# Optimization experiments

Measured on AMD Instinct MI355X. Metric: run time of the kernel, lower is better.

Reference implementation:

```python
import jax, jax.numpy as jnp
import numpy as np
from jax import lax

ALPHA = 4.0  # spikingjelly default Sigmoid surrogate alpha
EPS = 1e-5

@jax.custom_vjp
def spike_fn(u):
    return (u >= 0.0).astype(u.dtype)

def _spike_fwd(u):
    return spike_fn(u), u

def _spike_bwd(u, g):
    sg = jax.nn.sigmoid(ALPHA * u)
    return (g * ALPHA * sg * (1.0 - sg),)

spike_fn.defvjp(_spike_fwd, _spike_bwd)

def if_node(x):
    """Multi-step IF neuron (v_threshold=1, hard reset to 0) over leading T dim."""
    def step(v, xt):
        v = v + xt
        s = spike_fn(v - 1.0)
        v = v * (1.0 - s)
        return v, s
    _, spikes = lax.scan(step, jnp.zeros_like(x[0]), x)
    return spikes

def layer_norm(x, g, b):
    m = jnp.mean(x, axis=-1, keepdims=True)
    var = jnp.mean((x - m) ** 2, axis=-1, keepdims=True)
    return (x - m) * lax.rsqrt(var + EPS) * g + b

def setup_inputs() -> dict:
    key = jax.random.key(0)
    T, B, S, D = 4, 8, 1024, 768
    ks = jax.random.split(key, 5)
    scale = 1.0 / np.sqrt(D)
    inp = {
        "x": jax.random.normal(ks[0], (T, B, S, D), jnp.float32),
        "wq": jax.random.normal(ks[1], (D, D), jnp.float32) * scale,
        "wk": jax.random.normal(ks[2], (D, D), jnp.float32) * scale,
        "wv": jax.random.normal(ks[3], (D, D), jnp.float32) * scale,
        "wo": jax.random.normal(ks[4], (D, D), jnp.float32) * scale,
        "gq": jnp.ones((D,), jnp.float32), "bq": jnp.zeros((D,), jnp.float32),
        "gk": jnp.ones((D,), jnp.float32), "bk": jnp.zeros((D,), jnp.float32),
        "gv": jnp.ones((D,), jnp.float32), "bv": jnp.zeros((D,), jnp.float32),
        "go": jnp.ones((D,), jnp.float32), "bo": jnp.zeros((D,), jnp.float32),
    }
    return inp

def reference(x, wq, wk, wv, wo, gq, bq, gk, bk, gv, bv, go, bo):
    T, B, S, D = x.shape
    H, HD = 12, 64
    tmp = if_node(x)                                   # [T,B,S,D] spikes
    Q = if_node(layer_norm(tmp @ wq, gq, bq))
    K = if_node(layer_norm(tmp @ wk, gk, bk))
    V = if_node(layer_norm(tmp @ wv, gv, bv))
    # [T,B,S,H,HD] -> [T,B,H,S,HD]
    Q = Q.reshape(T, B, S, H, HD).transpose(0, 1, 3, 2, 4)
    K = K.reshape(T, B, S, H, HD).transpose(0, 1, 3, 2, 4)
    V = V.reshape(T, B, S, H, HD).transpose(0, 1, 3, 2, 4)
    QK = jnp.sum(Q * K, axis=-2, keepdims=True)        # [T,B,H,1,HD]
    QK = if_node(QK)                                   # talking_heads IF spikes
    QKV = V * QK                                       # broadcast over S
    QKV = QKV.transpose(0, 1, 3, 2, 4).reshape(T, B, S, D)
    return layer_norm(QKV @ wo, go, bo)
```

## Files before the change

### kernel.cpp

```cpp
#include <hip/hip_runtime.h>
#include <hip/hip_bf16.h>

#define T_ 4
#define B_ 8
#define S_ 1024
#define D_ 768
#define BS_ (B_*S_)
#define M_ (T_*B_*S_)
#define BSD_ (B_*S_*D_)
#define LN_EPS 1e-5f
#define TAU 4e-5f
#define TAU2 2e-6f
#define ECAP (1 << 20)

typedef unsigned short u16;
typedef unsigned char u8;
typedef unsigned int u32;
typedef unsigned long long u64;
typedef __bf16 bf16x8 __attribute__((ext_vector_type(8)));
typedef float f32x4 __attribute__((ext_vector_type(4)));

__global__ __launch_bounds__(768)
void k_if_mask(const float* __restrict__ x, u64* __restrict__ Am2) {
    int bs = blockIdx.x;
    int d = threadIdx.x;
    int wv = d >> 6, lane = d & 63;
    float v = 0.f;
    for (int t = 0; t < T_; ++t) {
        v += x[(size_t)t * BSD_ + (size_t)bs * D_ + d];
        bool s = (v >= 1.0f);
        u64 m = __ballot(s);
        if (lane == 0) Am2[((size_t)t * BS_ + bs) * 12 + wv] = m;
        if (s) v = 0.f;
    }
}

__global__ void k_wconv(const float* __restrict__ wq, const float* __restrict__ wk,
                        const float* __restrict__ wv, const float* __restrict__ wo,
                        u16* __restrict__ Whi, u16* __restrict__ Wlo, u16* __restrict__ Wo) {
    int idx = blockIdx.x * 256 + threadIdx.x;
    int mat = idx / (D_ * D_);
    int r = idx % (D_ * D_);
    int n = r / D_;
    int k = r % D_;
    const float* src = (mat == 0) ? wq : (mat == 1) ? wk : (mat == 2) ? wv : wo;
    float w = src[k * D_ + n];
    __bf16 hi = (__bf16)w;
    u16 uhi = __builtin_bit_cast(u16, hi);
    if (mat == 3) { Wo[r] = uhi; return; }
    float lo = w - (float)hi;
    u16 ulo = __builtin_bit_cast(u16, (__bf16)lo);
    Whi[(size_t)mat * D_ * D_ + r] = uhi;
    Wlo[(size_t)mat * D_ * D_ + r] = ulo;
}

__device__ __forceinline__ void gload16(const void* g, void* l) {
    __builtin_amdgcn_global_load_lds(
        (const __attribute__((address_space(1))) unsigned int*)g,
        (__attribute__((address_space(3))) unsigned int*)l, 16, 0, 0);
}

template<int NMATS, int KSTEP>
__global__ __launch_bounds__(256)
void k_gemm(const u64* __restrict__ Amask_g,
            const u16* __restrict__ Bh0, const u16* __restrict__ Bl0, float* __restrict__ C0,
            const u16* __restrict__ Bh1, const u16* __restrict__ Bl1, float* __restrict__ C1,
            const u16* __restrict__ Bh2, const u16* __restrict__ Bl2, float* __restrict__ C2,
            int ntn, int N) {
    constexpr int CH = KSTEP / 8;
    constexpr int CMASK = CH - 1;
    constexpr int NSUB = KSTEP / 32;
    constexpr int NW64 = KSTEP / 64;
    constexpr int NLOAD = KSTEP / 16;
    __shared__ __align__(16) u16 Bh[128 * KSTEP];
    __shared__ __align__(16) u16 Bl[NMATS == 2 ? 128 * KSTEP : 8];
    __shared__ __align__(16) u64 Amsk[128 * 13];
    __shared__ __align__(16) u32 LUT[256 * 4];
    int my = blockIdx.y;
    const u16* Bhi = (my == 0) ? Bh0 : (my == 1) ? Bh1 : Bh2;
    const u16* Blo = (my == 0) ? Bl0 : (my == 1) ? Bl1 : Bl2;
    float* C = (my == 0) ? C0 : (my == 1) ? C1 : C2;
    int bid = blockIdx.x;
    bid = (bid & 7) * (gridDim.x >> 3) + (bid >> 3);
    int bn = bid % ntn, bm = bid / ntn;
    int tid = threadIdx.x;
    int l = tid & 63, w = tid >> 6;
    int wr = w >> 1, wc = w & 1;
    int lan16 = l & 15, kh = l >> 4;

    {
        int e = tid;
        LUT[e * 4 + 0] = (((e >> 0) & 1) ? 0x3F80u : 0u) | (((e >> 1) & 1) ? 0x3F800000u : 0u);
        LUT[e * 4 + 1] = (((e >> 2) & 1) ? 0x3F80u : 0u) | (((e >> 3) & 1) ? 0x3F800000u : 0u);
        LUT[e * 4 + 2] = (((e >> 4) & 1) ? 0x3F80u : 0u) | (((e >> 5) & 1) ? 0x3F800000u : 0u);
        LUT[e * 4 + 3] = (((e >> 6) & 1) ? 0x3F80u : 0u) | (((e >> 7) & 1) ? 0x3F800000u : 0u);
    }
    #pragma unroll
    for (int j = 0; j < 6; ++j) {
        int idx = tid + j * 256;
        int r = idx / 12, kw = idx % 12;
        Amsk[r * 13 + kw] = Amask_g[(size_t)(bm * 128 + r) * 12 + kw];
    }

    f32x4 acc[4][4];
    #pragma unroll
    for (int m = 0; m < 4; ++m)
        #pragma unroll
        for (int n = 0; n < 4; ++n)
            #pragma unroll
            for (int r = 0; r < 4; ++r) acc[m][n][r] = 0.f;

    int srow[NLOAD], scol[NLOAD];
    #pragma unroll
    for (int j = 0; j < NLOAD; ++j) {
        int li = j * 256 + tid;
        srow[j] = li / CH;
        scol[j] = ((li & CMASK) ^ ((li / CH) & CMASK)) * 8;
    }
    int wbase = (tid >> 6) << 10;

    int arow[4], boff[4][NSUB];
    #pragma unroll
    for (int m = 0; m < 4; ++m) arow[m] = (wr * 64 + m * 16 + lan16) * 13;
    #pragma unroll
    for (int n = 0; n < 4; ++n)
        #pragma unroll
        for (int s = 0; s < NSUB; ++s) {
            int Rb = wc * 64 + n * 16 + lan16;
            boff[n][s] = Rb * (KSTEP * 2) + (((s * 4 + kh) ^ (Rb & CMASK)) << 4);
        }
    const char* LUTb = (const char*)LUT;

    for (int step = 0; step < 768 / KSTEP; ++step) {
        int kk = step * KSTEP;
        #pragma unroll
        for (int j = 0; j < NLOAD; ++j) {
            gload16(Bhi + (size_t)(bn * 128 + srow[j]) * 768 + kk + scol[j],
                    (char*)Bh + j * 4096 + wbase);
            if (NMATS == 2)
                gload16(Blo + (size_t)(bn * 128 + srow[j]) * 768 + kk + scol[j],
                        (char*)Bl + j * 4096 + wbase);
        }
        __syncthreads();
        u64 mA[4][NW64];
        #pragma unroll
        for (int m = 0; m < 4; ++m)
            #pragma unroll
            for (int ww = 0; ww < NW64; ++ww)
                mA[m][ww] = Amsk[arow[m] + step * NW64 + ww];
        #pragma unroll
        for (int s = 0; s < NSUB; ++s) {
            bf16x8 af[4], bh[4], bl[4];
            #pragma unroll
            for (int m = 0; m < 4; ++m) {
                int bitpos = s * 32;
                u64 mw = mA[m][bitpos >> 6];
                u32 byt = (u32)(mw >> ((bitpos & 63) + kh * 8)) & 0xFFu;
                af[m] = *(const bf16x8*)(LUTb + byt * 16);
            }
            #pragma unroll
            for (int n = 0; n < 4; ++n) {
                bh[n] = *(const bf16x8*)((const char*)Bh + boff[n][s]);
                if (NMATS == 2) bl[n] = *(const bf16x8*)((const char*)Bl + boff[n][s]);
            }
            #pragma unroll
            for (int m = 0; m < 4; ++m)
                #pragma unroll
                for (int n = 0; n < 4; ++n) {
                    acc[m][n] = __builtin_amdgcn_mfma_f32_16x16x32_bf16(af[m], bh[n], acc[m][n], 0, 0, 0);
                    if (NMATS == 2)
                        acc[m][n] = __builtin_amdgcn_mfma_f32_16x16x32_bf16(af[m], bl[n], acc[m][n], 0, 0, 0);
                }
        }
        __syncthreads();
    }
    #pragma unroll
    for (int m = 0; m < 4; ++m)
        #pragma unroll
        for (int n = 0; n < 4; ++n)
            #pragma unroll
            for (int r = 0; r < 4; ++r) {
                int crow = bm * 128 + wr * 64 + m * 16 + kh * 4 + r;
                int ccol = bn * 128 + wc * 64 + n * 16 + lan16;
                C[(size_t)crow * N + ccol] = acc[m][n][r];
            }
}

__global__ __launch_bounds__(256)
void k_lnif(const float* __restrict__ Y0, const float* __restrict__ Y1,
            const float* __restrict__ Y2,
            const float* __restrict__ gq, const float* __restrict__ bq,
            const float* __restrict__ gk, const float* __restrict__ bk,
            const float* __restrict__ gv, const float* __restrict__ bv,
            u8* __restrict__ Qs, u8* __restrict__ Ks, u8* __restrict__ Vs,
            float2* __restrict__ MI, u32* __restrict__ elist, int* __restrict__ ecnt,
            int mat0) {
    #pragma clang fp contract(off)
    int mat = mat0 + blockIdx.y;
    const float* Y = (mat == 0) ? Y0 : (mat == 1) ? Y1 : Y2;
    const float* g = (mat == 0) ? gq : (mat == 1) ? gk : gv;
    const float* bt = (mat == 0) ? bq : (mat == 1) ? bk : bv;
    u8* Sp = (mat == 0) ? Qs : (mat == 1) ? Ks : Vs;
    int row = blockIdx.x * 4 + (threadIdx.x >> 6);
    int lane = threadIdx.x & 63;
    float v[12];
    bool fl[12];
    #pragma unroll
    for (int i = 0; i < 12; ++i) { v[i] = 0.f; fl[i] = false; }
    float gv_[12], bv_[12];
    #pragma unroll
    for (int i = 0; i < 12; ++i) { gv_[i] = g[lane + 64*i]; bv_[i] = bt[lane + 64*i]; }
    for (int t = 0; t < T_; ++t) {
        size_t base = ((size_t)t * BS_ + row) * D_;
        float xv[12];
        double s = 0.0;
        #pragma unroll
        for (int i = 0; i < 12; ++i) { xv[i] = Y[base + lane + 64*i]; s += (double)xv[i]; }
        #pragma unroll
        for (int o = 1; o < 64; o <<= 1) s += __shfl_xor(s, o, 64);
        s = __shfl(s, 0, 64);
        float m = (float)(s / 768.0);
        float d[12];
        double q = 0.0;
        #pragma unroll
        for (int i = 0; i < 12; ++i) { d[i] = xv[i] - m; float sq = d[i]*d[i]; q += (double)sq; }
        #pragma unroll
        for (int o = 1; o < 64; o <<= 1) q += __shfl_xor(q, o, 64);
        q = __shfl(q, 0, 64);
        float var = (float)(q / 768.0);
        float inv = 1.0f / __fsqrt_rn(var + LN_EPS);
        if (lane == 0) MI[((size_t)mat * 4 + t) * BS_ + row] = make_float2(m, inv);
        #pragma unroll
        for (int i = 0; i < 12; ++i) {
            float yn = ((d[i] * inv) * gv_[i]) + bv_[i];
            v[i] += yn;
            fl[i] = fl[i] || (fabsf(v[i] - 1.0f) < TAU);
            bool sp = (v[i] >= 1.0f);
            Sp[base + lane + 64*i] = sp ? (u8)1 : (u8)0;
            if (sp) v[i] = 0.f;
        }
    }
    #pragma unroll
    for (int i = 0; i < 12; ++i) {
        if (fl[i]) {
            int slot = atomicAdd(ecnt, 1);
            if (slot < ECAP)
                elist[slot] = ((u32)mat << 23) | ((u32)row << 10) | (u32)(lane + 64*i);
        }
    }
}

__global__ __launch_bounds__(256)
void k_repair2(const u64* __restrict__ Am2,
               const float* __restrict__ wq, const float* __restrict__ wk,
               const float* __restrict__ wv, const float2* __restrict__ MI,
               const float* __restrict__ gq, const float* __restrict__ bq,
               const float* __restrict__ gk, const float* __restrict__ bk,
               const float* __restrict__ gv, const float* __restrict__ bv,
               u8* __restrict__ Qs, u8* __restrict__ Ks, u8* __restrict__ Vs,
               const u32* __restrict__ elist, const int* __restrict__ ecnt,
               int* __restrict__ rowlist2, int* __restrict__ cnt2) {
    #pragma clang fp contract(off)
    int nf = *ecnt;
    if (nf > ECAP) nf = ECAP;
    int t = threadIdx.x & 3;
    int gid = (blockIdx.x * 256 + threadIdx.x) >> 2;
    int ngroups = (gridDim.x * 256) >> 2;
    int lane = threadIdx.x & 63;
    int gbase = lane & ~3;
    for (int e = gid; e < nf; e += ngroups) {
        u32 p = elist[e];
        int mat = p >> 23;
        int row = (p >> 10) & 0x1FFF;
        int col = p & 0x3FF;
        const float* W = (mat == 0) ? wq : (mat == 1) ? wk : wv;
        const float* g = (mat == 0) ? gq : (mat == 1) ? gk : gv;
        const float* bb = (mat == 0) ? bq : (mat == 1) ? bk : bv;
        u8* Sp = (mat == 0) ? Qs : (mat == 1) ? Ks : Vs;
        float y = 0.f;
        for (int kw = 0; kw < 12; ++kw) {
            u64 m = Am2[((size_t)t * BS_ + row) * 12 + kw];
            const float* wp = W + (size_t)(kw * 64) * D_ + col;
            #pragma unroll 16
            for (int kb = 0; kb < 64; ++kb) {
                float w = wp[(size_t)kb * D_];
                y += ((m >> kb) & 1ull) ? w : 0.0f;
            }
        }
        float y0 = __shfl(y, gbase + 0, 64);
        float y1 = __shfl(y, gbase + 1, 64);
        float y2 = __shfl(y, gbase + 2, 64);
        float y3 = __shfl(y, gbase + 3, 64);
        float yt[4] = {y0, y1, y2, y3};
        float gc = g[col], bc = bb[col];
        float v = 0.f;
        bool efl = false;
        #pragma unroll
        for (int tt = 0; tt < 4; ++tt) {
            float2 mi = MI[((size_t)mat * 4 + tt) * BS_ + row];
            float yn = (((yt[tt] - mi.x) * mi.y) * gc) + bc;
            v += yn;
            efl = efl || (fabsf(v - 1.0f) < TAU2);
            bool sp = (v >= 1.0f);
            if (tt == t)
                Sp[((size_t)tt * BS_ + row) * D_ + col] = sp ? (u8)1 : (u8)0;
            if (sp) v = 0.f;
        }
        if (efl && t == 0) {
            int slot = atomicAdd(cnt2 + mat, 1);
            rowlist2[mat * BS_ + slot] = row;
        }
    }
}

__global__ __launch_bounds__(768)
void k_repairT(const u64* __restrict__ Am2,
               const float* __restrict__ wq, const float* __restrict__ wk,
               const float* __restrict__ wv,
               const float* __restrict__ gq, const float* __restrict__ bq,
               const float* __restrict__ gk, const float* __restrict__ bk,
               const float* __restrict__ gv, const float* __restrict__ bv,
               u8* __restrict__ Qs, u8* __restrict__ Ks, u8* __restrict__ Vs,
               const int* __restrict__ rowlist, const int* __restrict__ cnt) {
    #pragma clang fp contract(off)
    int mat = blockIdx.y;
    int nf = cnt[mat];
    const float* W = (mat == 0) ? wq : (mat == 1) ? wk : wv;
    const float* g = (mat == 0) ? gq : (mat == 1) ? gk : gv;
    const float* bb = (mat == 0) ? bq : (mat == 1) ? bk : bv;
    u8* Sp = (mat == 0) ? Qs : (mat == 1) ? Ks : Vs;
    const float4* Wv4 = (const float4*)W;

    __shared__ u64 mks[4][12];
    __shared__ int pops[4][12];
    __shared__ int cnt4[4];
    __shared__ u16 idxs[4][768];
    __shared__ float4 ys[4][192];
    __shared__ float2 mi_sh[4];
    __shared__ double redd[12];

    int tid = threadIdx.x;
    int t = tid / 192;
    int tg = tid % 192;

    for (int e = blockIdx.x; e < nf; e += gridDim.x) {
        int row = rowlist[mat * BS_ + e];

        if (tid < 48) {
            int tt = tid / 12, kw = tid % 12;
            u64 m = Am2[((size_t)tt * BS_ + row) * 12 + kw];
            mks[tt][kw] = m;
            pops[tt][kw] = __popcll(m);
        }
        __syncthreads();
        if (tid < 48) {
            int tt = tid / 12, kw = tid % 12;
            int off = 0;
            for (int j = 0; j < kw; ++j) off += pops[tt][j];
            u64 m = mks[tt][kw];
            int kb0 = kw * 64;
            while (m) {
                int kb = __builtin_ctzll(m);
                m &= m - 1;
                idxs[tt][off++] = (u16)(kb0 + kb);
            }
            if (kw == 11) cnt4[tt] = off;
        }
        __syncthreads();

        int cn = cnt4[t];
        float y0 = 0.f, y1 = 0.f, y2 = 0.f, y3 = 0.f;
        const u16* il = idxs[t];
        #pragma unroll 8
        for (int i = 0; i < cn; ++i) {
            float4 w = Wv4[(size_t)il[i] * 192 + tg];
            y0 += w.x; y1 += w.y; y2 += w.z; y3 += w.w;
        }

        int lane = tid & 63;
        int wv_t = tg >> 6;
        double s = (double)y0 + (double)y1 + (double)y2 + (double)y3;
        #pragma unroll
        for (int o = 1; o < 64; o <<= 1) s += __shfl_xor(s, o, 64);
        if (lane == 0) redd[t * 3 + wv_t] = s;
        __syncthreads();
        double stot = redd[t * 3] + redd[t * 3 + 1] + redd[t * 3 + 2];
        float mean = (float)(stot / 768.0);
        float d0 = y0 - mean, d1 = y1 - mean, d2 = y2 - mean, d3 = y3 - mean;
        double q = (double)(d0*d0) + (double)(d1*d1) + (double)(d2*d2) + (double)(d3*d3);
        #pragma unroll
        for (int o = 1; o < 64; o <<= 1) q += __shfl_xor(q, o, 64);
        __syncthreads();
        if (lane == 0) redd[t * 3 + wv_t] = q;
        __syncthreads();
        double qtot = redd[t * 3] + redd[t * 3 + 1] + redd[t * 3 + 2];
        float var = (float)(qtot / 768.0);
        float inv = 1.0f / __fsqrt_rn(var + LN_EPS);

        ys[t][tg] = make_float4(y0, y1, y2, y3);
        if (tg == 0) mi_sh[t] = make_float2(mean, inv);
        __syncthreads();

        if (tid < 192) {
            float4 gd = ((const float4*)g)[tg];
            float4 bd = ((const float4*)bb)[tg];
            float4 yt[4];
            float2 mi[4];
            #pragma unroll
            for (int tt = 0; tt < 4; ++tt) { yt[tt] = ys[tt][tg]; mi[tt] = mi_sh[tt]; }
            uchar4 o4[4];
            #pragma unroll
            for (int j = 0; j < 4; ++j) {
                float gj = (j == 0) ? gd.x : (j == 1) ? gd.y : (j == 2) ? gd.z : gd.w;
                float bj = (j == 0) ? bd.x : (j == 1) ? bd.y : (j == 2) ? bd.z : bd.w;
                float v = 0.f;
                #pragma unroll
                for (int tt = 0; tt < 4; ++tt) {
                    float yj = (j == 0) ? yt[tt].x : (j == 1) ? yt[tt].y : (j == 2) ? yt[tt].z : yt[tt].w;
                    float d = yj - mi[tt].x;
                    float yn = ((d * mi[tt].y) * gj) + bj;
                    v += yn;
                    bool sp = (v >= 1.0f);
                    u8 sb = sp ? (u8)1 : (u8)0;
                    if (j == 0) o4[tt].x = sb;
                    if (j == 1) o4[tt].y = sb;
                    if (j == 2) o4[tt].z = sb;
                    if (j == 3) o4[tt].w = sb;
                    if (sp) v = 0.f;
                }
            }
            #pragma unroll
            for (int tt = 0; tt < 4; ++tt)
                *(uchar4*)(Sp + ((size_t)tt * BS_ + row) * D_ + tg * 4) = o4[tt];
        }
        __syncthreads();
    }
}

__global__ void k_qkred(const u8* __restrict__ Q, const u8* __restrict__ K,
                        float* __restrict__ QK) {
    int bid = blockIdx.x;
    int sg = bid & 31, tb = bid >> 5;
    int tid = threadIdx.x;
    int c4 = tid * 4;
    size_t base = (size_t)tb * S_ * D_ + (size_t)sg * 32 * D_;
    int acc[4] = {0, 0, 0, 0};
    for (int s = 0; s < 32; ++s) {
        uchar4 q = *(const uchar4*)(Q + base + (size_t)s * D_ + c4);
        uchar4 k = *(const uchar4*)(K + base + (size_t)s * D_ + c4);
        acc[0] += q.x & k.x; acc[1] += q.y & k.y; acc[2] += q.z & k.z; acc[3] += q.w & k.w;
    }
    float* dst = QK + (size_t)tb * D_ + c4;
    #pragma unroll
    for (int j = 0; j < 4; ++j) atomicAdd(dst + j, (float)acc[j]);
}

__global__ __launch_bounds__(768)
void k_qkvm(const u8* __restrict__ Vs, const float* __restrict__ QK,
            u64* __restrict__ Am3) {
    int row = blockIdx.x;
    int d = threadIdx.x;
    int wv = d >> 6, lane = d & 63;
    int t = row >> 13;
    int b = (row & (BS_ - 1)) >> 10;
    float v = 0.f;
    u8 sp_t = 0;
    #pragma unroll
    for (int tt = 0; tt < T_; ++tt) {
        v += QK[tt * (B_ * D_) + b * D_ + d];
        bool s = (v >= 1.0f);
        if (tt == t) sp_t = s ? 1 : 0;
        if (s) v = 0.f;
    }
    u8 vv = Vs[(size_t)row * D_ + d] & sp_t;
    u64 m = __ballot(vv != 0);
    if (lane == 0) Am3[(size_t)row * 12 + wv] = m;
}

__device__ __forceinline__ float block_sum(float v, float* red) {
    #pragma unroll
    for (int o = 32; o > 0; o >>= 1) v += __shfl_down(v, o, 64);
    int lane = threadIdx.x & 63, w = threadIdx.x >> 6;
    __syncthreads();
    if (lane == 0) red[w] = v;
    __syncthreads();
    return (red[0] + red[1]) + (red[2] + red[3]);
}

__global__ __launch_bounds__(256)
void k_lnfinal(const float* __restrict__ Y, const float* __restrict__ g,
               const float* __restrict__ bt, float* __restrict__ out) {
    #pragma clang fp contract(off)
    __shared__ float red[4];
    size_t row = (size_t)blockIdx.x * D_;
    int tid = threadIdx.x;
    float y[3];
    float s = 0.f;
    #pragma unroll
    for (int j = 0; j < 3; ++j) { y[j] = Y[row + tid + j * 256]; s += y[j]; }
    float mean = block_sum(s, red) / 768.0f;
    float q = 0.f;
    #pragma unroll
    for (int j = 0; j < 3; ++j) { float d = y[j] - mean; q += d * d; }
    float var = block_sum(q, red) / 768.0f;
    float inv = 1.0f / __fsqrt_rn(var + LN_EPS);
    #pragma unroll
    for (int j = 0; j < 3; ++j) {
        int c = tid + j * 256;
        out[row + c] = (y[j] - mean) * inv * g[c] + bt[c];
    }
}

extern "C" void kernel_launch(void* const* d_in, const int* in_sizes, int n_in,
                              void* d_out, int out_size, void* d_ws, size_t ws_size,
                              hipStream_t stream) {
    const float* x  = (const float*)d_in[0];
    const float* wq = (const float*)d_in[1];
    const float* wk = (const float*)d_in[2];
    const float* wv = (const float*)d_in[3];
    const float* wo = (const float*)d_in[4];
    const float* gq = (const float*)d_in[5];
    const float* bq = (const float*)d_in[6];
    const float* gk = (const float*)d_in[7];
    const float* bk = (const float*)d_in[8];
    const float* gv = (const float*)d_in[9];
    const float* bv = (const float*)d_in[10];
    const float* go = (const float*)d_in[11];
    const float* bo = (const float*)d_in[12];
    float* out = (float*)d_out;

    char* ws = (char*)d_ws;
    size_t off = 0;
    auto alloc = [&](size_t bytes) -> void* {
        void* p = ws + off;
        off += (bytes + 255) & ~(size_t)255;
        return p;
    };
    u64* Am2   = (u64*)alloc((size_t)M_ * 12 * 8);
    u64* Am3   = (u64*)alloc((size_t)M_ * 12 * 8);
    float* Y0  = (float*)alloc((size_t)M_ * D_ * 4);
    u8* Qs     = (u8*)alloc((size_t)M_ * D_);
    u8* Ks     = (u8*)alloc((size_t)M_ * D_);
    u8* Vs     = (u8*)alloc((size_t)M_ * D_);
    u16* Whi   = (u16*)alloc((size_t)3 * D_ * D_ * 2);
    u16* Wlo   = (u16*)alloc((size_t)3 * D_ * D_ * 2);
    u16* Wo    = (u16*)alloc((size_t)D_ * D_ * 2);
    float* QK  = (float*)alloc((size_t)T_ * B_ * D_ * 4);
    float2* MI = (float2*)alloc((size_t)3 * 4 * BS_ * 8);
    u32* elist = (u32*)alloc((size_t)ECAP * 4);
    int* rowlist2 = (int*)alloc((size_t)3 * BS_ * 4);
    int* cnt   = (int*)alloc(256);
    float* Y1  = (float*)alloc((size_t)M_ * D_ * 4);
    float* Y2  = (float*)alloc((size_t)M_ * D_ * 4);
    bool fused = (off <= ws_size);
    if (!fused) { Y1 = Y0; Y2 = Y0; }
    int* cnt2 = cnt;
    int* ecnt = cnt + 3;

    hipMemsetAsync(QK, 0, (size_t)T_ * B_ * D_ * 4, stream);
    hipMemsetAsync(cnt, 0, 256, stream);

    k_if_mask<<<BS_, 768, 0, stream>>>(x, Am2);
    k_wconv<<<(4 * D_ * D_) / 256, 256, 0, stream>>>(wq, wk, wv, wo, Whi, Wlo, Wo);
    const int ntn = D_ / 128;
    const int gemm_grid = (M_ / 128) * ntn;
    const u16* WhiQ = Whi + 0 * D_ * D_; const u16* WloQ = Wlo + 0 * D_ * D_;
    const u16* WhiK = Whi + 1 * D_ * D_; const u16* WloK = Wlo + 1 * D_ * D_;
    const u16* WhiV = Whi + 2 * D_ * D_; const u16* WloV = Wlo + 2 * D_ * D_;
    if (fused) {
        k_gemm<2, 64><<<dim3(gemm_grid, 3), 256, 0, stream>>>(Am2,
            WhiQ, WloQ, Y0, WhiK, WloK, Y1, WhiV, WloV, Y2, ntn, D_);
        k_lnif<<<dim3(BS_ / 4, 3), 256, 0, stream>>>(Y0, Y1, Y2,
            gq, bq, gk, bk, gv, bv, Qs, Ks, Vs, MI, elist, ecnt, 0);
    } else {
        k_gemm<2, 64><<<dim3(gemm_grid, 1), 256, 0, stream>>>(Am2,
            WhiQ, WloQ, Y0, WhiQ, WloQ, Y0, WhiQ, WloQ, Y0, ntn, D_);
        k_lnif<<<dim3(BS_ / 4, 1), 256, 0, stream>>>(Y0, Y0, Y0,
            gq, bq, gk, bk, gv, bv, Qs, Ks, Vs, MI, elist, ecnt, 0);
        k_gemm<2, 64><<<dim3(gemm_grid, 1), 256, 0, stream>>>(Am2,
            WhiK, WloK, Y0, WhiK, WloK, Y0, WhiK, WloK, Y0, ntn, D_);
        k_lnif<<<dim3(BS_ / 4, 1), 256, 0, stream>>>(Y0, Y0, Y0,
            gq, bq, gk, bk, gv, bv, Qs, Ks, Vs, MI, elist, ecnt, 1);
        k_gemm<2, 64><<<dim3(gemm_grid, 1), 256, 0, stream>>>(Am2,
            WhiV, WloV, Y0, WhiV, WloV, Y0, WhiV, WloV, Y0, ntn, D_);
        k_lnif<<<dim3(BS_ / 4, 1), 256, 0, stream>>>(Y0, Y0, Y0,
            gq, bq, gk, bk, gv, bv, Qs, Ks, Vs, MI, elist, ecnt, 2);
    }
    k_repair2<<<512, 256, 0, stream>>>(Am2, wq, wk, wv, MI, gq, bq, gk, bk, gv, bv,
                                       Qs, Ks, Vs, elist, ecnt, rowlist2, cnt2);
    k_repairT<<<dim3(256, 3), 768, 0, stream>>>(Am2, wq, wk, wv, gq, bq, gk, bk, gv, bv,
                                                Qs, Ks, Vs, rowlist2, cnt2);
    k_qkred<<<T_ * B_ * 32, 192, 0, stream>>>(Qs, Ks, QK);
    k_qkvm<<<M_, 768, 0, stream>>>(Vs, QK, Am3);
    k_gemm<1, 128><<<dim3(gemm_grid, 1), 256, 0, stream>>>(Am3,
        Wo, Wo, Y0, Wo, Wo, Y0, Wo, Wo, Y0, ntn, D_);
    k_lnfinal<<<M_, 256, 0, stream>>>(Y0, go, bo, out);
}
```

Before: 584.5 us.

## Fuse QKV spike GEMM with layernorm and IF neuron in one kernel

Replaces the separate QKV GEMM plus layernorm/IF kernels with one kernel. Each block computes 64 rows (16 tokens × 4 timesteps, enabled by reordering the spike mask layout to token-major) across the full 768 columns. Row statistics and IF spiking are done in registers, so the three fp32 intermediate Y tensors are never written to or read back from global memory. The cost is a large LDS tile (96 KB for B), 512-thread blocks with heavy accumulator register use, and hi/lo weight passes run sequentially, which may lower occupancy.

```diff
diff --git a/kernel.cpp b/kernel.cpp
--- a/kernel.cpp
+++ b/kernel.cpp
@@ -30,7 +30,7 @@
         v += x[(size_t)t * BSD_ + (size_t)bs * D_ + d];
         bool s = (v >= 1.0f);
         u64 m = __ballot(s);
-        if (lane == 0) Am2[((size_t)t * BS_ + bs) * 12 + wv] = m;
+        if (lane == 0) Am2[((size_t)bs * 4 + t) * 12 + wv] = m;
         if (s) v = 0.f;
     }
 }
@@ -60,26 +60,216 @@
         (__attribute__((address_space(3))) unsigned int*)l, 16, 0, 0);
 }
 
-template<int NMATS, int KSTEP>
+__global__ __launch_bounds__(512)
+void k_gemmln(const u64* __restrict__ Am2,
+              const u16* __restrict__ Whi_all, const u16* __restrict__ Wlo_all,
+              const float* __restrict__ gq, const float* __restrict__ bq,
+              const float* __restrict__ gk, const float* __restrict__ bk,
+              const float* __restrict__ gv, const float* __restrict__ bv,
+              u8* __restrict__ Qs, u8* __restrict__ Ks, u8* __restrict__ Vs,
+              float2* __restrict__ MI, u32* __restrict__ elist, int* __restrict__ ecnt) {
+    #pragma clang fp contract(off)
+    __shared__ __align__(16) u16 Bt[768 * 64];
+    __shared__ __align__(16) u64 Amsk[64 * 13];
+    __shared__ __align__(16) u32 LUT[256 * 4];
+    __shared__ double red[64][4];
+    int mat = blockIdx.y;
+    const u16* Bhi = Whi_all + (size_t)mat * D_ * D_;
+    const u16* Blo = Wlo_all + (size_t)mat * D_ * D_;
+    const float* g = (mat == 0) ? gq : (mat == 1) ? gk : gv;
+    const float* bt = (mat == 0) ? bq : (mat == 1) ? bk : bv;
+    u8* Sp = (mat == 0) ? Qs : (mat == 1) ? Ks : Vs;
+
+    int bid = blockIdx.x;
+    bid = (bid & 7) * (gridDim.x >> 3) + (bid >> 3);
+    int bm = bid;
+    int tid = threadIdx.x;
+    int wid = tid >> 6, l = tid & 63;
+    int rh = wid >> 2, cq = wid & 3;
+    int lan16 = l & 15, kh = l >> 4;
+
+    if (tid < 256) {
+        int e = tid;
+        LUT[e * 4 + 0] = (((e >> 0) & 1) ? 0x3F80u : 0u) | (((e >> 1) & 1) ? 0x3F800000u : 0u);
+        LUT[e * 4 + 1] = (((e >> 2) & 1) ? 0x3F80u : 0u) | (((e >> 3) & 1) ? 0x3F800000u : 0u);
+        LUT[e * 4 + 2] = (((e >> 4) & 1) ? 0x3F80u : 0u) | (((e >> 5) & 1) ? 0x3F800000u : 0u);
+        LUT[e * 4 + 3] = (((e >> 6) & 1) ? 0x3F80u : 0u) | (((e >> 7) & 1) ? 0x3F800000u : 0u);
+    }
+    {
+        int idx = tid;
+        if (idx < 768) {
+            int r = idx / 12, kw = idx % 12;
+            Amsk[r * 13 + kw] = Am2[(size_t)(bm * 64 + r) * 12 + kw];
+        }
+        idx = tid + 512;
+        if (idx < 768) {
+            int r = idx / 12, kw = idx % 12;
+            Amsk[r * 13 + kw] = Am2[(size_t)(bm * 64 + r) * 12 + kw];
+        }
+    }
+
+    f32x4 acc[2][12];
+    #pragma unroll
+    for (int fm = 0; fm < 2; ++fm)
+        #pragma unroll
+        for (int fn = 0; fn < 12; ++fn)
+            #pragma unroll
+            for (int r = 0; r < 4; ++r) acc[fm][fn][r] = 0.f;
+
+    int srow[12], scol[12];
+    #pragma unroll
+    for (int j = 0; j < 12; ++j) {
+        int li = j * 512 + tid;
+        srow[j] = li >> 3;
+        scol[j] = ((li & 7) ^ ((li >> 3) & 7)) * 8;
+    }
+    int wbase = wid << 10;
+
+    int arow[2], boff[12][2];
+    #pragma unroll
+    for (int fm = 0; fm < 2; ++fm) arow[fm] = (rh * 32 + fm * 16 + lan16) * 13;
+    #pragma unroll
+    for (int fn = 0; fn < 12; ++fn)
+        #pragma unroll
+        for (int ss = 0; ss < 2; ++ss) {
+            int n = cq * 192 + fn * 16 + lan16;
+            boff[fn][ss] = n * 128 + (((ss * 4 + kh) ^ (n & 7)) << 4);
+        }
+    const char* LUTb = (const char*)LUT;
+
+    for (int step = 0; step < 24; ++step) {
+        bool hi = (step < 12);
+        int kk = (hi ? step : step - 12) * 64;
+        const u16* Bsrc = hi ? Bhi : Blo;
+        #pragma unroll
+        for (int j = 0; j < 12; ++j)
+            gload16(Bsrc + (size_t)srow[j] * 768 + kk + scol[j],
+                    (char*)Bt + j * 8192 + wbase);
+        __syncthreads();
+        u64 mw[2];
+        #pragma unroll
+        for (int fm = 0; fm < 2; ++fm) mw[fm] = Amsk[arow[fm] + (hi ? step : step - 12)];
+        #pragma unroll
+        for (int ss = 0; ss < 2; ++ss) {
+            bf16x8 af[2];
+            #pragma unroll
+            for (int fm = 0; fm < 2; ++fm) {
+                u32 byt = (u32)(mw[fm] >> (ss * 32 + kh * 8)) & 0xFFu;
+                af[fm] = *(const bf16x8*)(LUTb + byt * 16);
+            }
+            #pragma unroll
+            for (int fn = 0; fn < 12; ++fn) {
+                bf16x8 bf = *(const bf16x8*)((const char*)Bt + boff[fn][ss]);
+                acc[0][fn] = __builtin_amdgcn_mfma_f32_16x16x32_bf16(af[0], bf, acc[0][fn], 0, 0, 0);
+                acc[1][fn] = __builtin_amdgcn_mfma_f32_16x16x32_bf16(af[1], bf, acc[1][fn], 0, 0, 0);
+            }
+        }
+        __syncthreads();
+    }
+
+    double rs[2][4];
+    #pragma unroll
+    for (int fm = 0; fm < 2; ++fm)
+        #pragma unroll
+        for (int rg = 0; rg < 4; ++rg) {
+            double s = 0.0;
+            #pragma unroll
+            for (int fn = 0; fn < 12; ++fn) s += (double)acc[fm][fn][rg];
+            #pragma unroll
+            for (int o = 1; o < 16; o <<= 1) s += __shfl_xor(s, o, 64);
+            rs[fm][rg] = s;
+        }
+    if (lan16 == 0) {
+        #pragma unroll
+        for (int fm = 0; fm < 2; ++fm)
+            #pragma unroll
+            for (int rg = 0; rg < 4; ++rg)
+                red[rh * 32 + fm * 16 + kh * 4 + rg][cq] = rs[fm][rg];
+    }
+    __syncthreads();
+    float mean_[2][4];
+    #pragma unroll
+    for (int fm = 0; fm < 2; ++fm)
+        #pragma unroll
+        for (int rg = 0; rg < 4; ++rg) {
+            int R = rh * 32 + fm * 16 + kh * 4 + rg;
+            double stot = (red[R][0] + red[R][1]) + (red[R][2] + red[R][3]);
+            mean_[fm][rg] = (float)(stot / 768.0);
+        }
+    __syncthreads();
+    #pragma unroll
+    for (int fm = 0; fm < 2; ++fm)
+        #pragma unroll
+        for (int rg = 0; rg < 4; ++rg) {
+            double q = 0.0;
+            #pragma unroll
+            for (int fn = 0; fn < 12; ++fn) {
+                float d = acc[fm][fn][rg] - mean_[fm][rg];
+                float sq = d * d;
+                q += (double)sq;
+            }
+            #pragma unroll
+            for (int o = 1; o < 16; o <<= 1) q += __shfl_xor(q, o, 64);
+            rs[fm][rg] = q;
+        }
+    if (lan16 == 0) {
+        #pragma unroll
+        for (int fm = 0; fm < 2; ++fm)
+            #pragma unroll
+            for (int rg = 0; rg < 4; ++rg)
+                red[rh * 32 + fm * 16 + kh * 4 + rg][cq] = rs[fm][rg];
+    }
+    __syncthreads();
+    float inv_[2][4];
+    #pragma unroll
+    for (int fm = 0; fm < 2; ++fm)
+        #pragma unroll
+        for (int rg = 0; rg < 4; ++rg) {
+            int R = rh * 32 + fm * 16 + kh * 4 + rg;
+            double qtot = (red[R][0] + red[R][1]) + (red[R][2] + red[R][3]);
+            float var = (float)(qtot / 768.0);
+            inv_[fm][rg] = 1.0f / __fsqrt_rn(var + LN_EPS);
+        }
+
+    #pragma unroll
+    for (int fm = 0; fm < 2; ++fm) {
+        int bsg = bm * 16 + rh * 8 + fm * 4 + kh;
+        #pragma unroll
+        for (int fn = 0; fn < 12; ++fn) {
+            int col = cq * 192 + fn * 16 + lan16;
+            float gc = g[col], bc = bt[col];
+            float v = 0.f;
+            bool fl = false;
+            #pragma unroll
+            for (int t = 0; t < 4; ++t) {
+                float yn = ((acc[fm][fn][t] - mean_[fm][t]) * inv_[fm][t]) * gc + bc;
+                v += yn;
+                fl = fl || (fabsf(v - 1.0f) < TAU);
+                bool sp = (v >= 1.0f);
+                Sp[((size_t)t * BS_ + bsg) * D_ + col] = sp ? (u8)1 : (u8)0;
+                if (sp) v = 0.f;
+            }
+            if (fl) {
+                int slot = atomicAdd(ecnt, 1);
+                if (slot < ECAP)
+                    elist[slot] = ((u32)mat << 23) | ((u32)bsg << 10) | (u32)col;
+            }
+        }
+        if (lan16 == 0) {
+            #pragma unroll
+            for (int t = 0; t < 4; ++t)
+                MI[((size_t)mat * 4 + t) * BS_ + bsg] = make_float2(mean_[fm][t], inv_[fm][t]);
+        }
+    }
+}
+
 __global__ __launch_bounds__(256)
-void k_gemm(const u64* __restrict__ Amask_g,
-            const u16* __restrict__ Bh0, const u16* __restrict__ Bl0, float* __restrict__ C0,
-            const u16* __restrict__ Bh1, const u16* __restrict__ Bl1, float* __restrict__ C1,
-            const u16* __restrict__ Bh2, const u16* __restrict__ Bl2, float* __restrict__ C2,
-            int ntn, int N) {
-    constexpr int CH = KSTEP / 8;
-    constexpr int CMASK = CH - 1;
-    constexpr int NSUB = KSTEP / 32;
-    constexpr int NW64 = KSTEP / 64;
-    constexpr int NLOAD = KSTEP / 16;
+void k_gemmO(const u64* __restrict__ Amask_g, const u16* __restrict__ Bt_g,
+             float* __restrict__ C, int ntn, int N) {
+    constexpr int KSTEP = 128, CH = 16, CMASK = 15, NSUB = 4, NW64 = 2, NLOAD = 8;
     __shared__ __align__(16) u16 Bh[128 * KSTEP];
-    __shared__ __align__(16) u16 Bl[NMATS == 2 ? 128 * KSTEP : 8];
     __shared__ __align__(16) u64 Amsk[128 * 13];
     __shared__ __align__(16) u32 LUT[256 * 4];
-    int my = blockIdx.y;
-    const u16* Bhi = (my == 0) ? Bh0 : (my == 1) ? Bh1 : Bh2;
-    const u16* Blo = (my == 0) ? Bl0 : (my == 1) ? Bl1 : Bl2;
-    float* C = (my == 0) ? C0 : (my == 1) ? C1 : C2;
     int bid = blockIdx.x;
     bid = (bid & 7) * (gridDim.x >> 3) + (bid >> 3);
     int bn = bid % ntn, bm = bid / ntn;
@@ -87,7 +277,6 @@
     int l = tid & 63, w = tid >> 6;
     int wr = w >> 1, wc = w & 1;
     int lan16 = l & 15, kh = l >> 4;
-
     {
         int e = tid;
         LUT[e * 4 + 0] = (((e >> 0) & 1) ? 0x3F80u : 0u) | (((e >> 1) & 1) ? 0x3F800000u : 0u);
@@ -101,7 +290,6 @@
         int r = idx / 12, kw = idx % 12;
         Amsk[r * 13 + kw] = Amask_g[(size_t)(bm * 128 + r) * 12 + kw];
     }
-
     f32x4 acc[4][4];
     #pragma unroll
     for (int m = 0; m < 4; ++m)
@@ -109,7 +297,6 @@
         for (int n = 0; n < 4; ++n)
             #pragma unroll
             for (int r = 0; r < 4; ++r) acc[m][n][r] = 0.f;
-
     int srow[NLOAD], scol[NLOAD];
     #pragma unroll
     for (int j = 0; j < NLOAD; ++j) {
@@ -118,7 +305,6 @@
         scol[j] = ((li & CMASK) ^ ((li / CH) & CMASK)) * 8;
     }
     int wbase = (tid >> 6) << 10;
-
     int arow[4], boff[4][NSUB];
     #pragma unroll
     for (int m = 0; m < 4; ++m) arow[m] = (wr * 64 + m * 16 + lan16) * 13;
@@ -130,17 +316,12 @@
             boff[n][s] = Rb * (KSTEP * 2) + (((s * 4 + kh) ^ (Rb & CMASK)) << 4);
         }
     const char* LUTb = (const char*)LUT;
-
     for (int step = 0; step < 768 / KSTEP; ++step) {
         int kk = step * KSTEP;
         #pragma unroll
-        for (int j = 0; j < NLOAD; ++j) {
-            gload16(Bhi + (size_t)(bn * 128 + srow[j]) * 768 + kk + scol[j],
+        for (int j = 0; j < NLOAD; ++j)
+            gload16(Bt_g + (size_t)(bn * 128 + srow[j]) * 768 + kk + scol[j],
                     (char*)Bh + j * 4096 + wbase);
-            if (NMATS == 2)
-                gload16(Blo + (size_t)(bn * 128 + srow[j]) * 768 + kk + scol[j],
-                        (char*)Bl + j * 4096 + wbase);
-        }
         __syncthreads();
         u64 mA[4][NW64];
         #pragma unroll
@@ -150,27 +331,22 @@
                 mA[m][ww] = Amsk[arow[m] + step * NW64 + ww];
         #pragma unroll
         for (int s = 0; s < NSUB; ++s) {
-            bf16x8 af[4], bh[4], bl[4];
+            bf16x8 af[4], bh[4];
             #pragma unroll
             for (int m = 0; m < 4; ++m) {
                 int bitpos = s * 32;
-                u64 mw = mA[m][bitpos >> 6];
-                u32 byt = (u32)(mw >> ((bitpos & 63) + kh * 8)) & 0xFFu;
+                u64 mwv = mA[m][bitpos >> 6];
+                u32 byt = (u32)(mwv >> ((bitpos & 63) + kh * 8)) & 0xFFu;
                 af[m] = *(const bf16x8*)(LUTb + byt * 16);
             }
             #pragma unroll
-            for (int n = 0; n < 4; ++n) {
+            for (int n = 0; n < 4; ++n)
                 bh[n] = *(const bf16x8*)((const char*)Bh + boff[n][s]);
-                if (NMATS == 2) bl[n] = *(const bf16x8*)((const char*)Bl + boff[n][s]);
-            }
             #pragma unroll
             for (int m = 0; m < 4; ++m)
                 #pragma unroll
-                for (int n = 0; n < 4; ++n) {
+                for (int n = 0; n < 4; ++n)
                     acc[m][n] = __builtin_amdgcn_mfma_f32_16x16x32_bf16(af[m], bh[n], acc[m][n], 0, 0, 0);
-                    if (NMATS == 2)
-                        acc[m][n] = __builtin_amdgcn_mfma_f32_16x16x32_bf16(af[m], bl[n], acc[m][n], 0, 0, 0);
-                }
         }
         __syncthreads();
     }
@@ -184,70 +360,6 @@
                 int ccol = bn * 128 + wc * 64 + n * 16 + lan16;
                 C[(size_t)crow * N + ccol] = acc[m][n][r];
             }
-}
-
-__global__ __launch_bounds__(256)
-void k_lnif(const float* __restrict__ Y0, const float* __restrict__ Y1,
-            const float* __restrict__ Y2,
-            const float* __restrict__ gq, const float* __restrict__ bq,
-            const float* __restrict__ gk, const float* __restrict__ bk,
-            const float* __restrict__ gv, const float* __restrict__ bv,
-            u8* __restrict__ Qs, u8* __restrict__ Ks, u8* __restrict__ Vs,
-            float2* __restrict__ MI, u32* __restrict__ elist, int* __restrict__ ecnt,
-            int mat0) {
-    #pragma clang fp contract(off)
-    int mat = mat0 + blockIdx.y;
-    const float* Y = (mat == 0) ? Y0 : (mat == 1) ? Y1 : Y2;
-    const float* g = (mat == 0) ? gq : (mat == 1) ? gk : gv;
-    const float* bt = (mat == 0) ? bq : (mat == 1) ? bk : bv;
-    u8* Sp = (mat == 0) ? Qs : (mat == 1) ? Ks : Vs;
-    int row = blockIdx.x * 4 + (threadIdx.x >> 6);
-    int lane = threadIdx.x & 63;
-    float v[12];
-    bool fl[12];
-    #pragma unroll
-    for (int i = 0; i < 12; ++i) { v[i] = 0.f; fl[i] = false; }
-    float gv_[12], bv_[12];
-    #pragma unroll
-    for (int i = 0; i < 12; ++i) { gv_[i] = g[lane + 64*i]; bv_[i] = bt[lane + 64*i]; }
-    for (int t = 0; t < T_; ++t) {
-        size_t base = ((size_t)t * BS_ + row) * D_;
-        float xv[12];
-        double s = 0.0;
-        #pragma unroll
-        for (int i = 0; i < 12; ++i) { xv[i] = Y[base + lane + 64*i]; s += (double)xv[i]; }
-        #pragma unroll
-        for (int o = 1; o < 64; o <<= 1) s += __shfl_xor(s, o, 64);
-        s = __shfl(s, 0, 64);
-        float m = (float)(s / 768.0);
-        float d[12];
-        double q = 0.0;
-        #pragma unroll
-        for (int i = 0; i < 12; ++i) { d[i] = xv[i] - m; float sq = d[i]*d[i]; q += (double)sq; }
-        #pragma unroll
-        for (int o = 1; o < 64; o <<= 1) q += __shfl_xor(q, o, 64);
-        q = __shfl(q, 0, 64);
-        float var = (float)(q / 768.0);
-        float inv = 1.0f / __fsqrt_rn(var + LN_EPS);
-        if (lane == 0) MI[((size_t)mat * 4 + t) * BS_ + row] = make_float2(m, inv);
-        #pragma unroll
-        for (int i = 0; i < 12; ++i) {
-            float yn = ((d[i] * inv) * gv_[i]) + bv_[i];
-            v[i] += yn;
-            fl[i] = fl[i] || (fabsf(v[i] - 1.0f) < TAU);
-            bool sp = (v[i] >= 1.0f);
-            Sp[base + lane + 64*i] = sp ? (u8)1 : (u8)0;
-            if (sp) v[i] = 0.f;
-        }
-    }
-    #pragma unroll
-    for (int i = 0; i < 12; ++i) {
-        if (fl[i]) {
-            int slot = atomicAdd(ecnt, 1);
-            if (slot < ECAP)
-                elist[slot] = ((u32)mat << 23) | ((u32)row << 10) | (u32)(lane + 64*i);
-        }
-    }
 }
 
 __global__ __launch_bounds__(256)
@@ -279,7 +391,7 @@
         u8* Sp = (mat == 0) ? Qs : (mat == 1) ? Ks : Vs;
         float y = 0.f;
         for (int kw = 0; kw < 12; ++kw) {
-            u64 m = Am2[((size_t)t * BS_ + row) * 12 + kw];
+            u64 m = Am2[((size_t)row * 4 + t) * 12 + kw];
             const float* wp = W + (size_t)(kw * 64) * D_ + col;
             #pragma unroll 16
             for (int kb = 0; kb < 64; ++kb) {
@@ -348,7 +460,7 @@
 
         if (tid < 48) {
             int tt = tid / 12, kw = tid % 12;
-            u64 m = Am2[((size_t)tt * BS_ + row) * 12 + kw];
+            u64 m = Am2[((size_t)row * 4 + tt) * 12 + kw];
             mks[tt][kw] = m;
             pops[tt][kw] = __popcll(m);
         }
@@ -550,10 +662,6 @@
     u32* elist = (u32*)alloc((size_t)ECAP * 4);
     int* rowlist2 = (int*)alloc((size_t)3 * BS_ * 4);
     int* cnt   = (int*)alloc(256);
-    float* Y1  = (float*)alloc((size_t)M_ * D_ * 4);
-    float* Y2  = (float*)alloc((size_t)M_ * D_ * 4);
-    bool fused = (off <= ws_size);
-    if (!fused) { Y1 = Y0; Y2 = Y0; }
     int* cnt2 = cnt;
     int* ecnt = cnt + 3;
 
@@ -562,37 +670,14 @@
 
     k_if_mask<<<BS_, 768, 0, stream>>>(x, Am2);
     k_wconv<<<(4 * D_ * D_) / 256, 256, 0, stream>>>(wq, wk, wv, wo, Whi, Wlo, Wo);
-    const int ntn = D_ / 128;
-    const int gemm_grid = (M_ / 128) * ntn;
-    const u16* WhiQ = Whi + 0 * D_ * D_; const u16* WloQ = Wlo + 0 * D_ * D_;
-    const u16* WhiK = Whi + 1 * D_ * D_; const u16* WloK = Wlo + 1 * D_ * D_;
-    const u16* WhiV = Whi + 2 * D_ * D_; const u16* WloV = Wlo + 2 * D_ * D_;
-    if (fused) {
-        k_gemm<2, 64><<<dim3(gemm_grid, 3), 256, 0, stream>>>(Am2,
-            WhiQ, WloQ, Y0, WhiK, WloK, Y1, WhiV, WloV, Y2, ntn, D_);
-        k_lnif<<<dim3(BS_ / 4, 3), 256, 0, stream>>>(Y0, Y1, Y2,
-            gq, bq, gk, bk, gv, bv, Qs, Ks, Vs, MI, elist, ecnt, 0);
-    } else {
-        k_gemm<2, 64><<<dim3(gemm_grid, 1), 256, 0, stream>>>(Am2,
-            WhiQ, WloQ, Y0, WhiQ, WloQ, Y0, WhiQ, WloQ, Y0, ntn, D_);
-        k_lnif<<<dim3(BS_ / 4, 1), 256, 0, stream>>>(Y0, Y0, Y0,
-            gq, bq, gk, bk, gv, bv, Qs, Ks, Vs, MI, elist, ecnt, 0);
-        k_gemm<2, 64><<<dim3(gemm_grid, 1), 256, 0, stream>>>(Am2,
-            WhiK, WloK, Y0, WhiK, WloK, Y0, WhiK, WloK, Y0, ntn, D_);
-        k_lnif<<<dim3(BS_ / 4, 1), 256, 0, stream>>>(Y0, Y0, Y0,
-            gq, bq, gk, bk, gv, bv, Qs, Ks, Vs, MI, elist, ecnt, 1);
-        k_gemm<2, 64><<<dim3(gemm_grid, 1), 256, 0, stream>>>(Am2,
-            WhiV, WloV, Y0, WhiV, WloV, Y0, WhiV, WloV, Y0, ntn, D_);
-        k_lnif<<<dim3(BS_ / 4, 1), 256, 0, stream>>>(Y0, Y0, Y0,
-            gq, bq, gk, bk, gv, bv, Qs, Ks, Vs, MI, elist, ecnt, 2);
-    }
+    k_gemmln<<<dim3(M_ / 64, 3), 512, 0, stream>>>(Am2, Whi, Wlo,
+        gq, bq, gk, bk, gv, bv, Qs, Ks, Vs, MI, elist, ecnt);
     k_repair2<<<512, 256, 0, stream>>>(Am2, wq, wk, wv, MI, gq, bq, gk, bk, gv, bv,
                                        Qs, Ks, Vs, elist, ecnt, rowlist2, cnt2);
     k_repairT<<<dim3(256, 3), 768, 0, stream>>>(Am2, wq, wk, wv, gq, bq, gk, bk, gv, bv,
                                                 Qs, Ks, Vs, rowlist2, cnt2);
     k_qkred<<<T_ * B_ * 32, 192, 0, stream>>>(Qs, Ks, QK);
     k_qkvm<<<M_, 768, 0, stream>>>(Vs, QK, Am3);
-    k_gemm<1, 128><<<dim3(gemm_grid, 1), 256, 0, stream>>>(Am3,
-        Wo, Wo, Y0, Wo, Wo, Y0, Wo, Wo, Y0, ntn, D_);
+    k_gemmO<<<dim3((M_ / 128) * (D_ / 128), 1), 256, 0, stream>>>(Am3, Wo, Y0, D_ / 128, D_);
     k_lnfinal<<<M_, 256, 0, stream>>>(Y0, go, bo, out);
 }
```

Result: slower. 696.2 us (+19.1%).
